# Kernel optimization log

Hardware: AMD Instinct MI355X
Metric: run time of the kernel (lower is better)

Reference implementation:

```python
import jax, jax.numpy as jnp
import numpy as np

N_NODES = 100000
N_EDGES = 1600000
D = 64


def setup_inputs() -> dict:
    key = jax.random.key(0)
    k1, k2, k3 = jax.random.split(key, 3)
    z = jax.random.normal(k1, (N_NODES, D), dtype=jnp.float32)
    ei = jax.random.randint(k2, (2, N_EDGES), 0, N_NODES, dtype=jnp.int32)
    W = jax.random.normal(k3, (D, D), dtype=jnp.float32) * (1.0 / np.sqrt(D))
    b = jnp.zeros((D,), dtype=jnp.float32)
    return {"z": z, "ei": ei, "W": W, "b": b}


def reference(z, ei, W, b):
    # PyG GCNConv(64,64) with default add_self_loops=True, normalize=True, bias,
    # followed by ReLU (from StructDec.forward).
    N = z.shape[0]
    loops = jnp.arange(N, dtype=ei.dtype)
    src = jnp.concatenate([ei[0], loops])  # [E+N]
    dst = jnp.concatenate([ei[1], loops])  # [E+N]

    # symmetric normalization: deg computed on dst with unit edge weights
    deg = jax.ops.segment_sum(jnp.ones_like(dst, dtype=z.dtype), dst, num_segments=N)
    dinv = jnp.where(deg > 0, jax.lax.rsqrt(deg), 0.0)  # deg >= 1 due to self-loops
    norm = dinv[src] * dinv[dst]  # [E+N]

    # linear transform first (small GEMM), then gather-scale-scatter
    x = z @ W.T  # [N, D]
    msg = x[src] * norm[:, None]  # [E+N, D]
    out = jax.ops.segment_sum(msg, dst, num_segments=N) + b  # [N, D]
    return jax.nn.relu(out)
```

## Files before the change

kernel.cpp:

```cpp
#include <hip/hip_runtime.h>

#define DD 64
#define BSH 7
#define GBKT 128
#define CAP 2560
#define TILE 4096
#define PTHREADS 512
#define EPT 8
#define MAXBK 1024

__device__ __forceinline__ float bflo(unsigned int u) {
    return __uint_as_float(u << 16);
}
__device__ __forceinline__ float bfhi(unsigned int u) {
    return __uint_as_float(u & 0xffff0000u);
}
__device__ __forceinline__ unsigned short f2bf(float f) {
    unsigned int b = __float_as_uint(f);
    return (unsigned short)((b + 0x7fffu + ((b >> 16) & 1u)) >> 16);
}
__device__ __forceinline__ void acc_row(uint4 r, float4& lo, float4& hi) {
    lo.x += bflo(r.x); lo.y += bfhi(r.x);
    lo.z += bflo(r.y); lo.w += bfhi(r.y);
    hi.x += bflo(r.z); hi.y += bfhi(r.z);
    hi.z += bflo(r.w); hi.w += bfhi(r.w);
}

__global__ __launch_bounds__(PTHREADS) void part_k(const int* __restrict__ src,
                                                   const int* __restrict__ dst,
                                                   int* __restrict__ bcur,
                                                   int* __restrict__ bp,
                                                   int E, int NBK) {
    __shared__ int hist[MAXBK];
    __shared__ int scanb[MAXBK];
    __shared__ int gbase[MAXBK];
    __shared__ int stage[TILE];
    __shared__ unsigned short bstage[TILE];

    int tid = threadIdx.x;
    int tbase = blockIdx.x * TILE;
    int n = E - tbase;
    if (n > TILE) n = TILE;

    for (int i = tid; i < NBK; i += PTHREADS) hist[i] = 0;
    __syncthreads();

    int ss[EPT], dd[EPT];
    int eb = tid * EPT;
    bool dal = ((reinterpret_cast<size_t>(dst) & 15) == 0);
    if (dal && eb + EPT <= n) {
        const int4* s4 = (const int4*)(src + tbase + eb);
        const int4* d4 = (const int4*)(dst + tbase + eb);
        int4 a = s4[0], b2 = s4[1], c4 = d4[0], e4 = d4[1];
        ss[0] = a.x; ss[1] = a.y; ss[2] = a.z; ss[3] = a.w;
        ss[4] = b2.x; ss[5] = b2.y; ss[6] = b2.z; ss[7] = b2.w;
        dd[0] = c4.x; dd[1] = c4.y; dd[2] = c4.z; dd[3] = c4.w;
        dd[4] = e4.x; dd[5] = e4.y; dd[6] = e4.z; dd[7] = e4.w;
    } else {
        #pragma unroll
        for (int e = 0; e < EPT; ++e) {
            if (eb + e < n) { ss[e] = src[tbase + eb + e]; dd[e] = dst[tbase + eb + e]; }
            else dd[e] = -1;
        }
    }
    int pv[EPT], pb[EPT], pr[EPT];
    #pragma unroll
    for (int e = 0; e < EPT; ++e) {
        pb[e] = -1;
        if (eb + e < n && dd[e] >= 0) {
            pv[e] = (ss[e] << BSH) | (dd[e] & (GBKT - 1));
            pb[e] = dd[e] >> BSH;
            pr[e] = atomicAdd(&hist[pb[e]], 1);
        }
    }
    __syncthreads();

    if (tid < 64) {
        int run = 0;
        for (int base = 0; base < NBK; base += 64) {
            int i = base + tid;
            int orig = (i < NBK) ? hist[i] : 0;
            int v = orig;
            #pragma unroll
            for (int off = 1; off < 64; off <<= 1) {
                int t = __shfl_up(v, off, 64);
                if (tid >= off) v += t;
            }
            if (i < NBK) scanb[i] = run + v - orig;
            run += __shfl(v, 63, 64);
        }
    }
    __syncthreads();

    for (int i = tid; i < NBK; i += PTHREADS)
        if (hist[i]) gbase[i] = i * CAP + atomicAdd(&bcur[i], hist[i]);
    #pragma unroll
    for (int e = 0; e < EPT; ++e) {
        if (pb[e] >= 0) {
            int p = scanb[pb[e]] + pr[e];
            stage[p] = pv[e];
            bstage[p] = (unsigned short)pb[e];
        }
    }
    __syncthreads();

    for (int i = tid; i < n; i += PTHREADS) {
        int b = bstage[i];
        bp[gbase[b] + (i - scanb[b])] = stage[i];
    }
}

__global__ void nodedeg_k(const int* __restrict__ bp, const int* __restrict__ bcur,
                          float* __restrict__ dinv, int N) {
    __shared__ int cnt[GBKT];
    int k = blockIdx.x;
    int tid = threadIdx.x;
    int ebeg = k * CAP;
    int eend = ebeg + bcur[k];
    if (tid < GBKT) cnt[tid] = 0;
    __syncthreads();
    for (int i = ebeg + tid; i < eend; i += 256)
        atomicAdd(&cnt[bp[i] & (GBKT - 1)], 1);
    __syncthreads();
    if (tid < GBKT) {
        int node = (k << BSH) + tid;
        if (node < N) dinv[node] = rsqrtf((float)(1 + cnt[tid]));
    }
}

__global__ __launch_bounds__(512) void gemm_k(const float* __restrict__ z,
                                              const float* __restrict__ W,
                                              const float* __restrict__ dinv,
                                              ushort4* __restrict__ ybf, int N) {
    __shared__ float Wt[64 * 68];
    __shared__ float zt[32 * 68];
    int tid = threadIdx.x;
    for (int i = tid; i < DD * DD; i += 512) {
        int d = i >> 6, k = i & 63;
        Wt[k * 68 + d] = W[i];
    }
    {
        int zr = blockIdx.x * 32 + (tid >> 4);
        float4 v = (zr < N) ? reinterpret_cast<const float4*>(z)[(size_t)zr * 16 + (tid & 15)]
                            : make_float4(0.f, 0.f, 0.f, 0.f);
        *reinterpret_cast<float4*>(&zt[(tid >> 4) * 68 + (tid & 15) * 4]) = v;
    }
    __syncthreads();
    int r = tid >> 4;
    int c = tid & 15;
    int row = blockIdx.x * 32 + r;
    float4 acc = make_float4(0.f, 0.f, 0.f, 0.f);
    #pragma unroll
    for (int k = 0; k < DD; ++k) {
        float zv = zt[r * 68 + k];
        float4 w = *reinterpret_cast<const float4*>(&Wt[k * 68 + c * 4]);
        acc.x = fmaf(zv, w.x, acc.x);
        acc.y = fmaf(zv, w.y, acc.y);
        acc.z = fmaf(zv, w.z, acc.z);
        acc.w = fmaf(zv, w.w, acc.w);
    }
    if (row < N) {
        float s = dinv[row];
        ushort4 o;
        o.x = f2bf(acc.x * s);
        o.y = f2bf(acc.y * s);
        o.z = f2bf(acc.z * s);
        o.w = f2bf(acc.w * s);
        ybf[(size_t)row * 16 + c] = o;
    }
}

__global__ __launch_bounds__(256) void bg_k(const uint4* __restrict__ ybf,
                                            const int* __restrict__ bp,
                                            const int* __restrict__ bcur,
                                            const float4* __restrict__ b4,
                                            float4* __restrict__ out4, int N) {
    __shared__ int cnt[GBKT];
    __shared__ int excl[GBKT];
    __shared__ int cur[GBKT];
    __shared__ int sorted[CAP];
    __shared__ int nextn;
    int k = blockIdx.x;
    int tid = threadIdx.x;
    int ebeg = k * CAP;
    int eend = ebeg + bcur[k];
    int base = k << BSH;

    if (tid < GBKT) cnt[tid] = 0;
    if (tid == 0) nextn = 0;
    __syncthreads();
    int ev[10];
    #pragma unroll
    for (int u = 0; u < 10; ++u) {
        int i = ebeg + tid + u * 256;
        ev[u] = (i < eend) ? bp[i] : -1;
    }
    #pragma unroll
    for (int u = 0; u < 10; ++u)
        if (ev[u] >= 0) atomicAdd(&cnt[ev[u] & (GBKT - 1)], 1);
    __syncthreads();

    if (tid < GBKT) excl[tid] = cnt[tid];
    __syncthreads();
    #pragma unroll
    for (int off = 1; off < GBKT; off <<= 1) {
        int t = (tid < GBKT && tid >= off) ? excl[tid - off] : 0;
        __syncthreads();
        if (tid < GBKT) excl[tid] += t;
        __syncthreads();
    }
    if (tid < GBKT) {
        excl[tid] -= cnt[tid];
        cur[tid] = excl[tid];
    }
    __syncthreads();

    #pragma unroll
    for (int u = 0; u < 10; ++u)
        if (ev[u] >= 0) {
            int l = ev[u] & (GBKT - 1);
            int pos = atomicAdd(&cur[l], 1);
            sorted[pos] = ev[u] >> BSH;
        }
    __syncthreads();

    int lane = tid & 63;
    int c = tid & 7;
    for (;;) {
        int slot;
        if ((tid & 7) == 0) slot = atomicAdd(&nextn, 1);
        slot = __shfl(slot, lane & 56, 64);
        if (slot >= GBKT) break;
        int node = base + slot;
        if (node >= N) continue;
        int beg = excl[slot];
        int cn = cnt[slot];
        int end = beg + cn;
        uint4 v = ybf[(size_t)node * 8 + c];
        float4 a0 = make_float4(bflo(v.x), bfhi(v.x), bflo(v.y), bfhi(v.y));
        float4 a1 = make_float4(bflo(v.z), bfhi(v.z), bflo(v.w), bfhi(v.w));
        float4 e0 = make_float4(0.f, 0.f, 0.f, 0.f);
        float4 e1 = e0;
        int j = beg;
        for (; j + 7 < end; j += 8) {
            int s0 = sorted[j],     s1 = sorted[j + 1], s2 = sorted[j + 2], s3 = sorted[j + 3];
            int s4 = sorted[j + 4], s5 = sorted[j + 5], s6 = sorted[j + 6], s7 = sorted[j + 7];
            uint4 r0 = ybf[(size_t)s0 * 8 + c];
            uint4 r1 = ybf[(size_t)s1 * 8 + c];
            uint4 r2 = ybf[(size_t)s2 * 8 + c];
            uint4 r3 = ybf[(size_t)s3 * 8 + c];
            uint4 r4 = ybf[(size_t)s4 * 8 + c];
            uint4 r5 = ybf[(size_t)s5 * 8 + c];
            uint4 r6 = ybf[(size_t)s6 * 8 + c];
            uint4 r7 = ybf[(size_t)s7 * 8 + c];
            acc_row(r0, a0, a1);
            acc_row(r1, e0, e1);
            acc_row(r2, a0, a1);
            acc_row(r3, e0, e1);
            acc_row(r4, a0, a1);
            acc_row(r5, e0, e1);
            acc_row(r6, a0, a1);
            acc_row(r7, e0, e1);
        }
        for (; j + 3 < end; j += 4) {
            int s0 = sorted[j], s1 = sorted[j + 1], s2 = sorted[j + 2], s3 = sorted[j + 3];
            uint4 r0 = ybf[(size_t)s0 * 8 + c];
            uint4 r1 = ybf[(size_t)s1 * 8 + c];
            uint4 r2 = ybf[(size_t)s2 * 8 + c];
            uint4 r3 = ybf[(size_t)s3 * 8 + c];
            acc_row(r0, a0, a1);
            acc_row(r1, e0, e1);
            acc_row(r2, a0, a1);
            acc_row(r3, e0, e1);
        }
        for (; j < end; ++j) {
            uint4 r = ybf[(size_t)sorted[j] * 8 + c];
            acc_row(r, a0, a1);
        }
        a0.x += e0.x; a0.y += e0.y; a0.z += e0.z; a0.w += e0.w;
        a1.x += e1.x; a1.y += e1.y; a1.z += e1.z; a1.w += e1.w;

        float dn = rsqrtf((float)(1 + cn));
        float4 bb0 = b4[2 * c];
        float4 bb1 = b4[2 * c + 1];
        float4 o0, o1;
        o0.x = fmaxf(fmaf(a0.x, dn, bb0.x), 0.f);
        o0.y = fmaxf(fmaf(a0.y, dn, bb0.y), 0.f);
        o0.z = fmaxf(fmaf(a0.z, dn, bb0.z), 0.f);
        o0.w = fmaxf(fmaf(a0.w, dn, bb0.w), 0.f);
        o1.x = fmaxf(fmaf(a1.x, dn, bb1.x), 0.f);
        o1.y = fmaxf(fmaf(a1.y, dn, bb1.y), 0.f);
        o1.z = fmaxf(fmaf(a1.z, dn, bb1.z), 0.f);
        o1.w = fmaxf(fmaf(a1.w, dn, bb1.w), 0.f);
        out4[(size_t)node * 16 + 2 * c] = o0;
        out4[(size_t)node * 16 + 2 * c + 1] = o1;
    }
}


extern "C" void kernel_launch(void* const* d_in, const int* in_sizes, int n_in,
                              void* d_out, int out_size, void* d_ws, size_t ws_size,
                              hipStream_t stream) {
    const float* z = (const float*)d_in[0];
    const int* ei  = (const int*)d_in[1];
    const float* W = (const float*)d_in[2];
    const float* b = (const float*)d_in[3];
    float* out = (float*)d_out;

    const int N = in_sizes[0] / DD;
    const int E = in_sizes[1] / 2;
    const int* src = ei;
    const int* dst = ei + E;

    const int NBK = (N + GBKT - 1) >> BSH;

    unsigned short* ybf = (unsigned short*)d_ws;
    float* dinv  = (float*)(ybf + (size_t)64 * N);
    int*   bcur  = (int*)(dinv + N);
    int*   bp    = bcur + NBK;

    hipMemsetAsync(bcur, 0, sizeof(int) * NBK, stream);
    part_k<<<(E + TILE - 1) / TILE, PTHREADS, 0, stream>>>(src, dst, bcur, bp, E, NBK);
    nodedeg_k<<<NBK, 256, 0, stream>>>(bp, bcur, dinv, N);
    gemm_k<<<(N + 31) / 32, 512, 0, stream>>>(z, W, dinv, (ushort4*)ybf, N);
    bg_k<<<NBK, 256, 0, stream>>>((const uint4*)ybf, bp, bcur,
                                  (const float4*)b, (float4*)out, N);
}
```

Measured before the change: 92.30 us.

## Fuse degree count into GEMM kernel and double partition tile size

Merges the per-bucket degree counting kernel with the dense linear transform, so each 128-node bucket block computes dinv in shared memory and then transforms its 128 rows in four 32-row passes. This removes one launch and the global dinv round trip. The partition kernel also moves to 8192-element tiles with 1024 threads. The risk is fewer GEMM blocks (782 instead of 3125), each working serially, which lowers parallelism, and larger partition blocks that may reduce occupancy.

```diff
diff --git a/kernel.cpp b/kernel.cpp
--- a/kernel.cpp
+++ b/kernel.cpp
@@ -4,8 +4,8 @@
 #define BSH 7
 #define GBKT 128
 #define CAP 2560
-#define TILE 4096
-#define PTHREADS 512
+#define TILE 8192
+#define PTHREADS 1024
 #define EPT 8
 #define MAXBK 1024
 
@@ -110,63 +110,61 @@
     }
 }
 
-__global__ void nodedeg_k(const int* __restrict__ bp, const int* __restrict__ bcur,
-                          float* __restrict__ dinv, int N) {
+__global__ __launch_bounds__(512) void dg_k(const int* __restrict__ bp,
+                                            const int* __restrict__ bcur,
+                                            const float* __restrict__ z,
+                                            const float* __restrict__ W,
+                                            ushort4* __restrict__ ybf, int N) {
+    __shared__ float Wt[64 * 68];
+    __shared__ float zt[32 * 68];
     __shared__ int cnt[GBKT];
+    __shared__ float dinvL[GBKT];
     int k = blockIdx.x;
     int tid = threadIdx.x;
-    int ebeg = k * CAP;
-    int eend = ebeg + bcur[k];
+    int base = k << BSH;
+
     if (tid < GBKT) cnt[tid] = 0;
-    __syncthreads();
-    for (int i = ebeg + tid; i < eend; i += 256)
-        atomicAdd(&cnt[bp[i] & (GBKT - 1)], 1);
-    __syncthreads();
-    if (tid < GBKT) {
-        int node = (k << BSH) + tid;
-        if (node < N) dinv[node] = rsqrtf((float)(1 + cnt[tid]));
-    }
-}
-
-__global__ __launch_bounds__(512) void gemm_k(const float* __restrict__ z,
-                                              const float* __restrict__ W,
-                                              const float* __restrict__ dinv,
-                                              ushort4* __restrict__ ybf, int N) {
-    __shared__ float Wt[64 * 68];
-    __shared__ float zt[32 * 68];
-    int tid = threadIdx.x;
     for (int i = tid; i < DD * DD; i += 512) {
-        int d = i >> 6, k = i & 63;
-        Wt[k * 68 + d] = W[i];
-    }
+        int d = i >> 6, kk = i & 63;
+        Wt[kk * 68 + d] = W[i];
+    }
+    __syncthreads();
     {
-        int zr = blockIdx.x * 32 + (tid >> 4);
-        float4 v = (zr < N) ? reinterpret_cast<const float4*>(z)[(size_t)zr * 16 + (tid & 15)]
-                            : make_float4(0.f, 0.f, 0.f, 0.f);
-        *reinterpret_cast<float4*>(&zt[(tid >> 4) * 68 + (tid & 15) * 4]) = v;
-    }
-    __syncthreads();
-    int r = tid >> 4;
-    int c = tid & 15;
-    int row = blockIdx.x * 32 + r;
-    float4 acc = make_float4(0.f, 0.f, 0.f, 0.f);
-    #pragma unroll
-    for (int k = 0; k < DD; ++k) {
-        float zv = zt[r * 68 + k];
-        float4 w = *reinterpret_cast<const float4*>(&Wt[k * 68 + c * 4]);
-        acc.x = fmaf(zv, w.x, acc.x);
-        acc.y = fmaf(zv, w.y, acc.y);
-        acc.z = fmaf(zv, w.z, acc.z);
-        acc.w = fmaf(zv, w.w, acc.w);
-    }
-    if (row < N) {
-        float s = dinv[row];
-        ushort4 o;
-        o.x = f2bf(acc.x * s);
-        o.y = f2bf(acc.y * s);
-        o.z = f2bf(acc.z * s);
-        o.w = f2bf(acc.w * s);
-        ybf[(size_t)row * 16 + c] = o;
+        int ebeg = k * CAP;
+        int eend = ebeg + bcur[k];
+        for (int i = ebeg + tid; i < eend; i += 512)
+            atomicAdd(&cnt[bp[i] & (GBKT - 1)], 1);
+    }
+    __syncthreads();
+    if (tid < GBKT) dinvL[tid] = rsqrtf((float)(1 + cnt[tid]));
+    for (int it = 0; it < 4; ++it) {
+        __syncthreads();
+        int rl = it * 32 + (tid >> 4);
+        int row = base + rl;
+        float4 v = (row < N) ? ((const float4*)z)[(size_t)row * 16 + (tid & 15)]
+                             : make_float4(0.f, 0.f, 0.f, 0.f);
+        *(float4*)&zt[(tid >> 4) * 68 + (tid & 15) * 4] = v;
+        __syncthreads();
+        int r = tid >> 4, c = tid & 15;
+        float4 acc = make_float4(0.f, 0.f, 0.f, 0.f);
+        #pragma unroll
+        for (int kk = 0; kk < DD; ++kk) {
+            float zv = zt[r * 68 + kk];
+            float4 w = *(const float4*)&Wt[kk * 68 + c * 4];
+            acc.x = fmaf(zv, w.x, acc.x);
+            acc.y = fmaf(zv, w.y, acc.y);
+            acc.z = fmaf(zv, w.z, acc.z);
+            acc.w = fmaf(zv, w.w, acc.w);
+        }
+        if (row < N) {
+            float s = dinvL[rl];
+            ushort4 o;
+            o.x = f2bf(acc.x * s);
+            o.y = f2bf(acc.y * s);
+            o.z = f2bf(acc.z * s);
+            o.w = f2bf(acc.w * s);
+            ybf[(size_t)row * 16 + c] = o;
+        }
     }
 }
 
@@ -315,14 +313,12 @@
     const int NBK = (N + GBKT - 1) >> BSH;
 
     unsigned short* ybf = (unsigned short*)d_ws;
-    float* dinv  = (float*)(ybf + (size_t)64 * N);
-    int*   bcur  = (int*)(dinv + N);
+    int*   bcur  = (int*)(ybf + (size_t)64 * N);
     int*   bp    = bcur + NBK;
 
     hipMemsetAsync(bcur, 0, sizeof(int) * NBK, stream);
     part_k<<<(E + TILE - 1) / TILE, PTHREADS, 0, stream>>>(src, dst, bcur, bp, E, NBK);
-    nodedeg_k<<<NBK, 256, 0, stream>>>(bp, bcur, dinv, N);
-    gemm_k<<<(N + 31) / 32, 512, 0, stream>>>(z, W, dinv, (ushort4*)ybf, N);
+    dg_k<<<NBK, 512, 0, stream>>>(bp, bcur, z, W, (ushort4*)ybf, N);
     bg_k<<<NBK, 256, 0, stream>>>((const uint4*)ybf, bp, bcur,
                                   (const float4*)b, (float4*)out, N);
 }
```

Result: faster. 87.33 us, median of 2 (-5.4%).
